# Kernel tuning notes

Measured on AMD Instinct MI355X. Metric: run time of the kernel, lower is better.

The kernel has to match this reference:

```python
import jax, jax.numpy as jnp
import numpy as np
from jax import lax

B, CIN, D = 1, 32, 80      # batch, input channels (diffusion volumes), cube side
CE, CH, COUT = 64, 256, 6  # encoding feats, hidden feats, output feats (DTI components)
N = 200000                 # number of masked voxels
K = 3                      # FOVin


def _conv3d(x, w, b):
    # x: [B,C,D,H,W], w: [O,I,3,3,3], zero padding 1 (matches Conv3d(k=3, pad=1))
    y = lax.conv_general_dilated(x, w, window_strides=(1, 1, 1),
                                 padding=[(K // 2, K // 2)] * 3,
                                 dimension_numbers=('NCDHW', 'OIDHW', 'NCDHW'))
    return y + b[None, :, None, None, None]


def _conv1x1(x, w, b):
    # pointwise Conv1d: x [B,C,N], w [O,C], b [O]
    return jnp.einsum('oc,bcn->bon', w, x) + b[None, :, None]


def setup_inputs() -> dict:
    key = jax.random.key(0)
    ks = jax.random.split(key, 16)
    s3 = 1.0 / np.sqrt(CIN * K ** 3)
    return {
        'img_block': jax.random.normal(ks[0], (B, CIN, D, D, D), jnp.float32),
        'coords0': jax.random.randint(ks[1], (1, N), 0, D, jnp.int32),
        'coords1': jax.random.randint(ks[2], (1, N), 0, D, jnp.int32),
        'coords2': jax.random.randint(ks[3], (1, N), 0, D, jnp.int32),
        # encoder Conv3d weights (kaiming-ish scale)
        'w_enc1': jax.random.normal(ks[4], (CE, CIN, K, K, K), jnp.float32) * s3,
        'b_enc1': jax.random.normal(ks[5], (CE,), jnp.float32) * 0.01,
        'w_enc2': jax.random.normal(ks[6], (CE, CE, K, K, K), jnp.float32) * (1.0 / np.sqrt(CE * K ** 3)),
        'b_enc2': jax.random.normal(ks[7], (CE,), jnp.float32) * 0.01,
        # process stack 1x1 Conv1d weights
        'w_p1': jax.random.normal(ks[8], (CH, CE), jnp.float32) * (1.0 / np.sqrt(CE)),
        'b_p1': jax.random.normal(ks[9], (CH,), jnp.float32) * 0.01,
        'w_p2': jax.random.normal(ks[10], (CH, CH), jnp.float32) * (1.0 / np.sqrt(CH)),
        'b_p2': jax.random.normal(ks[11], (CH,), jnp.float32) * 0.01,
        'w_p3': jax.random.normal(ks[12], (64, CH), jnp.float32) * (1.0 / np.sqrt(CH)),
        'b_p3': jax.random.normal(ks[13], (64,), jnp.float32) * 0.01,
        'w_p4': jax.random.normal(ks[14], (COUT, 64), jnp.float32) * (1.0 / np.sqrt(64)),
        'b_p4': jax.random.normal(ks[15], (COUT,), jnp.float32) * 0.01,
    }


def reference(img_block, coords0, coords1, coords2,
              w_enc1, b_enc1, w_enc2, b_enc2,
              w_p1, b_p1, w_p2, b_p2, w_p3, b_p3, w_p4, b_p4):
    relu = jax.nn.relu
    # net_extrafea: two Conv3d(k=3,pad=1)+ReLU
    f = relu(_conv3d(img_block, w_enc1, b_enc1))
    f = relu(_conv3d(f, w_enc2, b_enc2))          # [B, CE, D, D, D]
    # gather masked voxels -> [B, CE, N]
    g = f[:, :, coords0[0], coords1[0], coords2[0]]
    # net_process (Dropout = identity in eval mode):
    h = relu(_conv1x1(g, w_p1, b_p1))             # [B, CH, N]
    h = relu(_conv1x1(h, w_p2, b_p2))             # [B, CH, N]
    # outermost_linear head: Conv1d(CH->64) then Conv1d(64->COUT), no nonlinearity
    h = _conv1x1(h, w_p3, b_p3)                   # [B, 64, N]
    out = _conv1x1(h, w_p4, b_p4)                 # [B, COUT, N]
    return out
```

## Files before the change

### kernel.cpp

```cpp
#include <hip/hip_runtime.h>
#include <hip/hip_bf16.h>

#define DD 80
#define CIN 32
#define PLANE (DD*DD)
#define VOX (DD*DD*DD)
#define NPTS 200000

typedef __attribute__((ext_vector_type(8))) short bf16x8;
typedef __attribute__((ext_vector_type(4))) float floatx4;
typedef __attribute__((ext_vector_type(4))) short s4v;

static __device__ __forceinline__ short f2bf(float v) {
    __hip_bfloat16 b = __float2bfloat16(v);
    return *(short*)&b;
}

static __device__ __forceinline__ void async_copy16(void* lds, const void* g) {
    __builtin_amdgcn_global_load_lds(
        (const __attribute__((address_space(1))) unsigned int*)g,
        (__attribute__((address_space(3))) unsigned int*)lds, 16, 0, 0);
}

__global__ void convert_weights(const float* __restrict__ w2,
                                const float* __restrict__ w_p1,
                                const float* __restrict__ w_p2,
                                const float* __restrict__ w_p3,
                                const float* __restrict__ w_e1,
                                short* __restrict__ wpb, short* __restrict__ w1f,
                                short* __restrict__ w2f, short* __restrict__ w3f,
                                short* __restrict__ wc1) {
    int i = blockIdx.x * 256 + threadIdx.x;
    if (i < 110592) {
        int off = i >> 12, r = i & 4095;
        int nt = r >> 10, r2 = r & 1023;
        int ks = r2 >> 9, r3 = r2 & 511;
        int lane = r3 >> 3, e = r3 & 7;
        int oc = nt * 16 + (lane & 15);
        int ic = ks * 32 + (lane >> 4) * 8 + e;
        wpb[i] = f2bf(w2[oc * 1728 + ic * 27 + off]);
    } else if (i < 110592 + 16384) {
        int j = i - 110592;
        int frag = j >> 9, r3 = j & 511;
        int lane = r3 >> 3, e = r3 & 7;
        int ks = frag & 1, nt = (frag >> 1) & 3, w = frag >> 3;
        int n = w * 64 + nt * 16 + (lane & 15);
        int k = ks * 32 + (lane >> 4) * 8 + e;
        w1f[j] = f2bf(w_p1[n * 64 + k]);
    } else if (i < 110592 + 16384 + 65536) {
        int j = i - 110592 - 16384;
        int frag = j >> 9, r3 = j & 511;
        int lane = r3 >> 3, e = r3 & 7;
        int ks = frag & 7, nt = (frag >> 3) & 3, w = frag >> 5;
        int n = w * 64 + nt * 16 + (lane & 15);
        int k = ks * 32 + (lane >> 4) * 8 + e;
        w2f[j] = f2bf(w_p2[n * 256 + k]);
    } else if (i < 110592 + 16384 + 65536 + 16384) {
        int j = i - 110592 - 16384 - 65536;
        int frag = j >> 9, r3 = j & 511;
        int lane = r3 >> 3, e = r3 & 7;
        int ks = frag & 7, w = frag >> 3;
        int n = w * 16 + (lane & 15);
        int k = ks * 32 + (lane >> 4) * 8 + e;
        w3f[j] = f2bf(w_p3[n * 256 + k]);
    } else if (i < 110592 + 16384 + 65536 + 16384 + 55296) {
        int j = i - (110592 + 16384 + 65536 + 16384);
        int off = j / 2048, r = j - off * 2048;
        int oc = r >> 5, ic = r & 31;
        wc1[j] = f2bf(w_e1[(oc * 32 + ic) * 27 + off]);
    }
}

__global__ __launch_bounds__(256) void transpose_img(
    const float* __restrict__ img, short* __restrict__ img_t)
{
    int v = blockIdx.x * 256 + threadIdx.x;
    if (v >= VOX) return;
    short row[32];
    #pragma unroll
    for (int ic = 0; ic < 32; ic++)
        row[ic] = f2bf(img[(size_t)ic * VOX + v]);
    int4* dst = (int4*)(img_t + (size_t)v * 32);
    #pragma unroll
    for (int c = 0; c < 4; c++) dst[c] = ((int4*)row)[c];
}

__global__ __launch_bounds__(256) void conv1_mfma(
    const short* __restrict__ img_t, const short* __restrict__ wc1,
    const float* __restrict__ b1, const short* __restrict__ zeros,
    short* __restrict__ f1)
{
    __shared__ short Alds[3072 * 16 / 2];

    const int bh = blockIdx.x;
    const int d = bh / DD, h = bh - d * DD;
    const int tid = threadIdx.x;
    const int w = tid >> 6, lane = tid & 63;
    const int q = lane >> 4, lc = lane & 15;

    for (int i = 0; i < 12; i++) {
        int s = (w * 12 + i) * 64 + lane;
        int row = s >> 2, c = s & 3;
        int cs = c ^ ((row >> 1) & 3);
        int rr = row / 82, v = row - rr * 82;
        int dz = rr / 3, dyy = rr - dz * 3;
        int zz = d + dz - 1, yy = h + dyy - 1, ww = v - 1;
        const short* src = zeros;
        if (row < 738 && (unsigned)zz < DD && (unsigned)yy < DD && (unsigned)ww < DD)
            src = img_t + ((size_t)(zz * PLANE + yy * DD + ww)) * 32 + cs * 8;
        async_copy16(&Alds[(w * 12 + i) * 512], src);
    }
    __syncthreads();

    floatx4 acc[5];
    #pragma unroll
    for (int mt = 0; mt < 5; mt++) acc[mt] = (floatx4){0.f, 0.f, 0.f, 0.f};

    for (int dz = 0; dz < 3; dz++) {
        for (int dy = 0; dy < 3; dy++) {
            const int rr = dz * 3 + dy;
            #pragma unroll
            for (int dx = 0; dx < 3; dx++) {
                const int off = rr * 3 + dx;
                bf16x8 bfr = *(const bf16x8*)(wc1 + ((off * 64 + w * 16 + lc) << 5) + q * 8);
                #pragma unroll
                for (int mt = 0; mt < 5; mt++) {
                    const int vv = rr * 82 + mt * 16 + lc + dx;
                    bf16x8 afr = *(const bf16x8*)(
                        &Alds[vv * 32 + ((q ^ ((vv >> 1) & 3)) << 3)]);
                    acc[mt] = __builtin_amdgcn_mfma_f32_16x16x32_bf16(afr, bfr, acc[mt], 0, 0, 0);
                }
            }
        }
    }

    const int oc = w * 16 + lc;
    const float bias = b1[oc];
    const size_t vbase = (size_t)(d * DD + h) * DD;
    #pragma unroll
    for (int mt = 0; mt < 5; mt++) {
        #pragma unroll
        for (int r = 0; r < 4; r++) {
            const int m = mt * 16 + q * 4 + r;
            float v = acc[mt][r] + bias;
            f1[(vbase + m) * 64 + oc] = f2bf(v > 0.f ? v : 0.f);
        }
    }
}

#define NSB 32

__global__ __launch_bounds__(512) void hist_cells(
    const int* __restrict__ c0, const int* __restrict__ c1, const int* __restrict__ c2,
    int* __restrict__ partial)
{
    __shared__ int h[1000];
    const int tid = threadIdx.x;
    for (int c = tid; c < 1000; c += 512) h[c] = 0;
    __syncthreads();
    for (int p = blockIdx.x * 512 + tid; p < NPTS; p += NSB * 512) {
        int cell = (c0[p] >> 3) * 100 + (c1[p] >> 3) * 10 + (c2[p] >> 3);
        atomicAdd(&h[cell], 1);
    }
    __syncthreads();
    for (int c = tid; c < 1000; c += 512) partial[c * NSB + blockIdx.x] = h[c];
}

__global__ __launch_bounds__(1024) void scan_cells(
    const int* __restrict__ partial, int* __restrict__ blockbase,
    int* __restrict__ cs, int* __restrict__ ce)
{
    __shared__ int a[1024], b[1024];
    const int t = threadIdx.x;
    int sum = 0;
    if (t < 1000) {
        const int base = t * NSB;
        int run = 0;
        #pragma unroll 8
        for (int bb = 0; bb < NSB; bb++) {
            blockbase[base + bb] = run;
            run += partial[base + bb];
        }
        sum = run;
    }
    a[t] = sum;
    __syncthreads();
    int* src = a; int* dst = b;
    for (int d = 1; d < 1024; d <<= 1) {
        int v = src[t];
        if (t >= d) v += src[t - d];
        dst[t] = v;
        __syncthreads();
        int* tmp = src; src = dst; dst = tmp;
    }
    if (t < 1000) { cs[t] = src[t] - sum; ce[t] = src[t]; }
}

__global__ __launch_bounds__(512) void scatter_points(
    const int* __restrict__ c0, const int* __restrict__ c1, const int* __restrict__ c2,
    const int* __restrict__ cs, const int* __restrict__ blockbase,
    int* __restrict__ perm, int* __restrict__ pcoord)
{
    __shared__ int cur[1000];
    const int tid = threadIdx.x;
    for (int c = tid; c < 1000; c += 512) cur[c] = 0;
    __syncthreads();
    for (int p = blockIdx.x * 512 + tid; p < NPTS; p += NSB * 512) {
        int z = c0[p], y = c1[p], x = c2[p];
        int cell = (z >> 3) * 100 + (y >> 3) * 10 + (x >> 3);
        int r = atomicAdd(&cur[cell], 1);
        int pos = cs[cell] + blockbase[cell * NSB + blockIdx.x] + r;
        perm[pos] = p;
        pcoord[pos] = z | (y << 8) | (x << 16);
    }
}

__global__ __launch_bounds__(512) void conv2_halo(
    const short* __restrict__ f1s, const short* __restrict__ wfb,
    const float* __restrict__ b2,
    const int* __restrict__ cs, const int* __restrict__ ce,
    const int* __restrict__ perm, const int* __restrict__ pcoord,
    const short* __restrict__ zeros,
    __hip_bfloat16* __restrict__ g)
{
    __shared__ short Alds[1000 * 64];

    int bid = blockIdx.x;
    { const int xcd = bid & 7, i = bid >> 3; bid = xcd * 125 + i; }
    const int cell = bid;
    const int cz = cell / 100, cyx = cell - cz * 100;
    const int cy = cyx / 10, cx = cyx - cy * 10;

    const int tid = threadIdx.x;
    const int w = tid >> 6, lane = tid & 63;
    const int q = lane >> 4, lc = lane & 15;

    const int pstart = cs[cell], pend = ce[cell];

    const int pr = lane >> 3, pcs = lane & 7, ccs = pcs ^ pr;
    const int gz0 = cz * 8 - 1, gy0 = cy * 8 - 1, gx0 = cx * 8 - 1;
    for (int j = w; j < 125; j += 8) {
        int r = j * 8 + pr;
        int hz = r / 100; int rem = r - hz * 100;
        int hy = rem / 10; int hx = rem - hy * 10;
        int gz = gz0 + hz, gy = gy0 + hy, gx = gx0 + hx;
        const short* src = zeros + ccs * 8;
        if ((unsigned)gz < DD && (unsigned)gy < DD && (unsigned)gx < DD)
            src = f1s + (size_t)(gz * PLANE + gy * DD + gx) * 64 + ccs * 8;
        async_copy16(&Alds[j * 512], src);
    }
    asm volatile("s_waitcnt vmcnt(0)" ::: "memory");
    __syncthreads();

    float bias[4];
    #pragma unroll
    for (int nt = 0; nt < 4; nt++) bias[nt] = b2[nt * 16 + lc];

    for (int pb2 = pstart; pb2 < pend; pb2 += 256) {
        int hbase[2];
        #pragma unroll
        for (int mt = 0; mt < 2; mt++) {
            int p = pb2 + w * 32 + mt * 16 + lc;
            if (p >= pend) p = pend - 1;
            int pk = pcoord[p];
            int z = pk & 0xff, y = (pk >> 8) & 0xff, x = (pk >> 16) & 0xff;
            hbase[mt] = (z - gz0) * 100 + (y - gy0) * 10 + (x - gx0);
        }

        floatx4 acc[2][4];
        #pragma unroll
        for (int mt = 0; mt < 2; mt++)
            #pragma unroll
            for (int nt = 0; nt < 4; nt++)
                acc[mt][nt] = (floatx4){0.f, 0.f, 0.f, 0.f};

        #pragma unroll 3
        for (int off = 0; off < 27; ++off) {
            const int dz = off / 9, rem = off - dz * 9;
            const int dy = rem / 3, dx = rem - dy * 3;
            const int dh = (dz - 1) * 100 + (dy - 1) * 10 + (dx - 1);

            bf16x8 bfr[4][2];
            #pragma unroll
            for (int nt = 0; nt < 4; nt++)
                #pragma unroll
                for (int ks = 0; ks < 2; ks++)
                    bfr[nt][ks] = *(const bf16x8*)(
                        wfb + off * 4096 + nt * 1024 + ks * 512 + lane * 8);

            bf16x8 afr[2][2];
            #pragma unroll
            for (int mt = 0; mt < 2; mt++) {
                const int hrow = hbase[mt] + dh;
                const int sw = hrow & 7;
                #pragma unroll
                for (int ks = 0; ks < 2; ks++)
                    afr[mt][ks] = *(const bf16x8*)(
                        &Alds[hrow * 64 + (((ks * 4 + q) ^ sw) << 3)]);
            }

            #pragma unroll
            for (int ks = 0; ks < 2; ks++)
                #pragma unroll
                for (int mt = 0; mt < 2; mt++)
                    #pragma unroll
                    for (int nt = 0; nt < 4; nt++)
                        acc[mt][nt] = __builtin_amdgcn_mfma_f32_16x16x32_bf16(
                            afr[mt][ks], bfr[nt][ks], acc[mt][nt], 0, 0, 0);
        }

        #pragma unroll
        for (int mt = 0; mt < 2; mt++) {
            const int pt = pb2 + w * 32 + mt * 16 + q * 4;
            #pragma unroll
            for (int r = 0; r < 4; r++) {
                if (pt + r < pend) {
                    const int orig = perm[pt + r];
                    #pragma unroll
                    for (int nt = 0; nt < 4; nt++) {
                        const int oc = nt * 16 + lc;
                        float v = acc[mt][nt][r] + bias[nt];
                        g[(size_t)orig * 64 + oc] = __float2bfloat16(v > 0.f ? v : 0.f);
                    }
                }
            }
        }
    }
}

__global__ __launch_bounds__(256) void mlp_mfma(
    const __hip_bfloat16* __restrict__ g,
    const short* __restrict__ w1f, const float* __restrict__ bp1,
    const short* __restrict__ w2f, const float* __restrict__ bp2,
    const short* __restrict__ w3f, const float* __restrict__ bp3,
    const float* __restrict__ wp4, const float* __restrict__ bp4,
    float* __restrict__ out)
{
    __shared__ short Xls[64 * 64];
    __shared__ short Hb[2][64 * 256];
    float* h3f = (float*)Hb[0];

    const int tid = threadIdx.x;
    const int pb = blockIdx.x * 64;
    const int w = tid >> 6, lane = tid & 63;
    const int q = lane >> 4, lc = lane & 15;

    const short* gs = (const short*)g;
    #pragma unroll
    for (int it = 0; it < 2; it++) {
        int idx = it * 256 + tid;
        int r = idx >> 3, c = idx & 7;
        int4 v = *(const int4*)(gs + (size_t)(pb + r) * 64 + c * 8);
        *(int4*)(&Xls[r * 64 + (c ^ (r & 7)) * 8]) = v;
    }
    __syncthreads();

    {
        floatx4 acc[4][4];
        #pragma unroll
        for (int mt = 0; mt < 4; mt++)
            #pragma unroll
            for (int nt = 0; nt < 4; nt++)
                acc[mt][nt] = (floatx4){0.f, 0.f, 0.f, 0.f};

        #pragma unroll
        for (int ks = 0; ks < 2; ks++) {
            bf16x8 wf[4];
            #pragma unroll
            for (int nt = 0; nt < 4; nt++)
                wf[nt] = *(const bf16x8*)(w1f + (((w * 4 + nt) * 2 + ks) << 9) + lane * 8);
            const int c = ks * 4 + q;
            #pragma unroll
            for (int mt = 0; mt < 4; mt++) {
                const int m = mt * 16 + lc;
                bf16x8 hf = *(const bf16x8*)(&Xls[m * 64 + ((c ^ (m & 7)) << 3)]);
                #pragma unroll
                for (int nt = 0; nt < 4; nt++)
                    acc[mt][nt] = __builtin_amdgcn_mfma_f32_16x16x32_bf16(wf[nt], hf, acc[mt][nt], 0, 0, 0);
            }
        }
        #pragma unroll
        for (int nt = 0; nt < 4; nt++) {
            const floatx4 bs = *(const floatx4*)(bp1 + w * 64 + nt * 16 + q * 4);
            const int chunk = w * 8 + nt * 2 + (q >> 1);
            #pragma unroll
            for (int mt = 0; mt < 4; mt++) {
                const int m = mt * 16 + lc;
                s4v hv;
                #pragma unroll
                for (int r = 0; r < 4; r++) {
                    float v = acc[mt][nt][r] + bs[r];
                    hv[r] = f2bf(v > 0.f ? v : 0.f);
                }
                *(s4v*)(&Hb[0][m * 256 + ((chunk ^ (m & 7)) << 3) + ((q & 1) << 2)]) = hv;
            }
        }
    }
    __syncthreads();

    {
        floatx4 acc[4][4];
        #pragma unroll
        for (int mt = 0; mt < 4; mt++)
            #pragma unroll
            for (int nt = 0; nt < 4; nt++)
                acc[mt][nt] = (floatx4){0.f, 0.f, 0.f, 0.f};

        #pragma unroll
        for (int ks = 0; ks < 8; ks++) {
            bf16x8 wf[4];
            #pragma unroll
            for (int nt = 0; nt < 4; nt++)
                wf[nt] = *(const bf16x8*)(w2f + (((w * 4 + nt) * 8 + ks) << 9) + lane * 8);
            const int c = ks * 4 + q;
            #pragma unroll
            for (int mt = 0; mt < 4; mt++) {
                const int m = mt * 16 + lc;
                bf16x8 hf = *(const bf16x8*)(&Hb[0][m * 256 + ((c ^ (m & 7)) << 3)]);
                #pragma unroll
                for (int nt = 0; nt < 4; nt++)
                    acc[mt][nt] = __builtin_amdgcn_mfma_f32_16x16x32_bf16(wf[nt], hf, acc[mt][nt], 0, 0, 0);
            }
        }
        #pragma unroll
        for (int nt = 0; nt < 4; nt++) {
            const floatx4 bs = *(const floatx4*)(bp2 + w * 64 + nt * 16 + q * 4);
            const int chunk = w * 8 + nt * 2 + (q >> 1);
            #pragma unroll
            for (int mt = 0; mt < 4; mt++) {
                const int m = mt * 16 + lc;
                s4v hv;
                #pragma unroll
                for (int r = 0; r < 4; r++) {
                    float v = acc[mt][nt][r] + bs[r];
                    hv[r] = f2bf(v > 0.f ? v : 0.f);
                }
                *(s4v*)(&Hb[1][m * 256 + ((chunk ^ (m & 7)) << 3) + ((q & 1) << 2)]) = hv;
            }
        }
    }
    __syncthreads();

    {
        floatx4 acc3[4];
        #pragma unroll
        for (int mt = 0; mt < 4; mt++) acc3[mt] = (floatx4){0.f, 0.f, 0.f, 0.f};

        #pragma unroll
        for (int ks = 0; ks < 8; ks++) {
            bf16x8 wf = *(const bf16x8*)(w3f + (((w * 8 + ks)) << 9) + lane * 8);
            const int c = ks * 4 + q;
            #pragma unroll
            for (int mt = 0; mt < 4; mt++) {
                const int m = mt * 16 + lc;
                bf16x8 hf = *(const bf16x8*)(&Hb[1][m * 256 + ((c ^ (m & 7)) << 3)]);
                acc3[mt] = __builtin_amdgcn_mfma_f32_16x16x32_bf16(wf, hf, acc3[mt], 0, 0, 0);
            }
        }
        const floatx4 bs = *(const floatx4*)(bp3 + w * 16 + q * 4);
        __syncthreads();
        #pragma unroll
        for (int mt = 0; mt < 4; mt++) {
            const int m = mt * 16 + lc;
            floatx4 hv;
            #pragma unroll
            for (int r = 0; r < 4; r++) hv[r] = acc3[mt][r] + bs[r];
            *(floatx4*)(&h3f[m * 68 + w * 16 + q * 4]) = hv;
        }
    }
    __syncthreads();

    for (int e = tid; e < 384; e += 256) {
        int c = e >> 6, p = e & 63;
        float a = bp4[c];
        const float* wr = wp4 + c * 64;
        const float* xr = h3f + p * 68;
        #pragma unroll 8
        for (int k = 0; k < 64; k++) a += wr[k] * xr[k];
        out[(size_t)c * NPTS + pb + p] = a;
    }
}

extern "C" void kernel_launch(void* const* d_in, const int* in_sizes, int n_in,
                              void* d_out, int out_size, void* d_ws, size_t ws_size,
                              hipStream_t stream) {
    const float* img = (const float*)d_in[0];
    const int* c0 = (const int*)d_in[1];
    const int* c1 = (const int*)d_in[2];
    const int* c2 = (const int*)d_in[3];
    const float* w_enc1 = (const float*)d_in[4];
    const float* b_enc1 = (const float*)d_in[5];
    const float* w_enc2 = (const float*)d_in[6];
    const float* b_enc2 = (const float*)d_in[7];
    const float* w_p1 = (const float*)d_in[8];
    const float* b_p1 = (const float*)d_in[9];
    const float* w_p2 = (const float*)d_in[10];
    const float* b_p2 = (const float*)d_in[11];
    const float* w_p3 = (const float*)d_in[12];
    const float* b_p3 = (const float*)d_in[13];
    const float* w_p4 = (const float*)d_in[14];
    const float* b_p4 = (const float*)d_in[15];
    float* out = (float*)d_out;

    short* f1b = (short*)d_ws;
    short* wpb = f1b + (size_t)VOX * 64;
    short* w1b = wpb + 110592;
    short* w2b = w1b + 16384;
    short* w3b = w2b + 65536;
    short* gb  = w3b + 16384;
    short* img_t = gb + (size_t)NPTS * 64;
    short* wc1 = img_t + (size_t)VOX * 32;
    short* zeros = wc1 + 55296;

    int* perm      = (int*)img_t;
    int* pcoord    = perm + NPTS;
    int* partial   = pcoord + NPTS;
    int* blockbase = partial + NSB * 1000;
    int* cstart    = blockbase + NSB * 1000;
    int* cend      = cstart + 1000;

    hipMemsetAsync(zeros, 0, 128, stream);
    convert_weights<<<(264192 + 255) / 256, 256, 0, stream>>>(
        w_enc2, w_p1, w_p2, w_p3, w_enc1, wpb, w1b, w2b, w3b, wc1);
    transpose_img<<<(VOX + 255) / 256, 256, 0, stream>>>(img, img_t);
    conv1_mfma<<<DD * DD, 256, 0, stream>>>(img_t, wc1, b_enc1, zeros, f1b);

    hist_cells<<<NSB, 512, 0, stream>>>(c0, c1, c2, partial);
    scan_cells<<<1, 1024, 0, stream>>>(partial, blockbase, cstart, cend);
    scatter_points<<<NSB, 512, 0, stream>>>(c0, c1, c2, cstart, blockbase, perm, pcoord);

    conv2_halo<<<1000, 512, 0, stream>>>(
        f1b, wpb, b_enc2, cstart, cend, perm, pcoord, zeros, (__hip_bfloat16*)gb);
    mlp_mfma<<<NPTS / 64, 256, 0, stream>>>(
        (const __hip_bfloat16*)gb, w1b, b_p1, w2b, b_p2, w3b, b_p3, w_p4, b_p4, out);
}
```

Before: 377.6 us.

## Fuse conv2 halo kernel with MLP stack, reusing shared memory per cell

Merges the sparse conv2 kernel and the pointwise MLP into one per-cell kernel. The conv2 outputs stay in LDS as MLP inputs and final results are scattered to the original point indices through perm, so the bf16 intermediate g never goes to global memory and one launch is removed. Because LDS is shared between the halo tile and the MLP buffers, the halo is reloaded for every 256-point chunk. Per-cell work becomes serialized with many barriers, and cells with many points pay for repeated halo loads. The MFMA operand order in conv2 is swapped to fit the new output layout.

Result: slower. 409.7 us (+8.5%).

```diff
diff --git a/kernel.cpp b/kernel.cpp
--- a/kernel.cpp
+++ b/kernel.cpp
@@ -215,15 +215,24 @@
     }
 }
 
-__global__ __launch_bounds__(512) void conv2_halo(
+__global__ __launch_bounds__(512) void conv2_mlp_fused(
     const short* __restrict__ f1s, const short* __restrict__ wfb,
     const float* __restrict__ b2,
     const int* __restrict__ cs, const int* __restrict__ ce,
     const int* __restrict__ perm, const int* __restrict__ pcoord,
     const short* __restrict__ zeros,
-    __hip_bfloat16* __restrict__ g)
+    const short* __restrict__ w1f, const float* __restrict__ bp1,
+    const short* __restrict__ w2f, const float* __restrict__ bp2,
+    const short* __restrict__ w3f, const float* __restrict__ bp3,
+    const float* __restrict__ wp4, const float* __restrict__ bp4,
+    float* __restrict__ out)
 {
-    __shared__ short Alds[1000 * 64];
+    __shared__ short U[64000];
+    short* Alds = U;
+    short* Xg = U;
+    short* H1 = U + 16384;
+    short* H2 = U + 32768;
+    float* h3f = (float*)H1;
 
     int bid = blockIdx.x;
     { const int xcd = bid & 7, i = bid >> 3; bid = xcd * 125 + i; }
@@ -236,27 +245,23 @@
     const int q = lane >> 4, lc = lane & 15;
 
     const int pstart = cs[cell], pend = ce[cell];
-
     const int pr = lane >> 3, pcs = lane & 7, ccs = pcs ^ pr;
     const int gz0 = cz * 8 - 1, gy0 = cy * 8 - 1, gx0 = cx * 8 - 1;
-    for (int j = w; j < 125; j += 8) {
-        int r = j * 8 + pr;
-        int hz = r / 100; int rem = r - hz * 100;
-        int hy = rem / 10; int hx = rem - hy * 10;
-        int gz = gz0 + hz, gy = gy0 + hy, gx = gx0 + hx;
-        const short* src = zeros + ccs * 8;
-        if ((unsigned)gz < DD && (unsigned)gy < DD && (unsigned)gx < DD)
-            src = f1s + (size_t)(gz * PLANE + gy * DD + gx) * 64 + ccs * 8;
-        async_copy16(&Alds[j * 512], src);
-    }
-    asm volatile("s_waitcnt vmcnt(0)" ::: "memory");
-    __syncthreads();
-
-    float bias[4];
-    #pragma unroll
-    for (int nt = 0; nt < 4; nt++) bias[nt] = b2[nt * 16 + lc];
 
     for (int pb2 = pstart; pb2 < pend; pb2 += 256) {
+        for (int j = w; j < 125; j += 8) {
+            int r = j * 8 + pr;
+            int hz = r / 100; int rem = r - hz * 100;
+            int hy = rem / 10; int hx = rem - hy * 10;
+            int gz = gz0 + hz, gy = gy0 + hy, gx = gx0 + hx;
+            const short* src = zeros + ccs * 8;
+            if ((unsigned)gz < DD && (unsigned)gy < DD && (unsigned)gx < DD)
+                src = f1s + (size_t)(gz * PLANE + gy * DD + gx) * 64 + ccs * 8;
+            async_copy16(&Alds[j * 512], src);
+        }
+        asm volatile("s_waitcnt vmcnt(0)" ::: "memory");
+        __syncthreads();
+
         int hbase[2];
         #pragma unroll
         for (int mt = 0; mt < 2; mt++) {
@@ -274,210 +279,206 @@
             for (int nt = 0; nt < 4; nt++)
                 acc[mt][nt] = (floatx4){0.f, 0.f, 0.f, 0.f};
 
-        #pragma unroll 3
-        for (int off = 0; off < 27; ++off) {
-            const int dz = off / 9, rem = off - dz * 9;
-            const int dy = rem / 3, dx = rem - dy * 3;
-            const int dh = (dz - 1) * 100 + (dy - 1) * 10 + (dx - 1);
-
-            bf16x8 bfr[4][2];
+        if (pb2 + w * 32 < pend) {
+            for (int dz = 0; dz < 3; dz++) {
+                for (int dy = 0; dy < 3; dy++) {
+                    const int rowoff = (dz - 1) * 100 + (dy - 1) * 10;
+                    const int offbase = (dz * 3 + dy) * 3;
+                    #pragma unroll
+                    for (int dx = 0; dx < 3; dx++) {
+                        const int off = offbase + dx;
+                        const int dh = rowoff + dx - 1;
+
+                        bf16x8 bfr[4][2];
+                        #pragma unroll
+                        for (int nt = 0; nt < 4; nt++)
+                            #pragma unroll
+                            for (int ks = 0; ks < 2; ks++)
+                                bfr[nt][ks] = *(const bf16x8*)(
+                                    wfb + off * 4096 + nt * 1024 + ks * 512 + lane * 8);
+
+                        bf16x8 afr[2][2];
+                        #pragma unroll
+                        for (int mt = 0; mt < 2; mt++) {
+                            const int hrow = hbase[mt] + dh;
+                            const int sw = hrow & 7;
+                            #pragma unroll
+                            for (int ks = 0; ks < 2; ks++)
+                                afr[mt][ks] = *(const bf16x8*)(
+                                    &Alds[hrow * 64 + (((ks * 4 + q) ^ sw) << 3)]);
+                        }
+
+                        #pragma unroll
+                        for (int ks = 0; ks < 2; ks++)
+                            #pragma unroll
+                            for (int mt = 0; mt < 2; mt++)
+                                #pragma unroll
+                                for (int nt = 0; nt < 4; nt++)
+                                    acc[mt][nt] = __builtin_amdgcn_mfma_f32_16x16x32_bf16(
+                                        bfr[nt][ks], afr[mt][ks], acc[mt][nt], 0, 0, 0);
+                    }
+                }
+            }
+        }
+        __syncthreads();
+
+        {
+            short* Xw = Xg + (w >> 1) * 4096;
             #pragma unroll
-            for (int nt = 0; nt < 4; nt++)
-                #pragma unroll
-                for (int ks = 0; ks < 2; ks++)
-                    bfr[nt][ks] = *(const bf16x8*)(
-                        wfb + off * 4096 + nt * 1024 + ks * 512 + lane * 8);
-
-            bf16x8 afr[2][2];
-            #pragma unroll
-            for (int mt = 0; mt < 2; mt++) {
-                const int hrow = hbase[mt] + dh;
-                const int sw = hrow & 7;
-                #pragma unroll
-                for (int ks = 0; ks < 2; ks++)
-                    afr[mt][ks] = *(const bf16x8*)(
-                        &Alds[hrow * 64 + (((ks * 4 + q) ^ sw) << 3)]);
-            }
-
-            #pragma unroll
-            for (int ks = 0; ks < 2; ks++)
-                #pragma unroll
-                for (int mt = 0; mt < 2; mt++)
-                    #pragma unroll
-                    for (int nt = 0; nt < 4; nt++)
-                        acc[mt][nt] = __builtin_amdgcn_mfma_f32_16x16x32_bf16(
-                            afr[mt][ks], bfr[nt][ks], acc[mt][nt], 0, 0, 0);
-        }
-
-        #pragma unroll
-        for (int mt = 0; mt < 2; mt++) {
-            const int pt = pb2 + w * 32 + mt * 16 + q * 4;
-            #pragma unroll
-            for (int r = 0; r < 4; r++) {
-                if (pt + r < pend) {
-                    const int orig = perm[pt + r];
-                    #pragma unroll
-                    for (int nt = 0; nt < 4; nt++) {
-                        const int oc = nt * 16 + lc;
-                        float v = acc[mt][nt][r] + bias[nt];
-                        g[(size_t)orig * 64 + oc] = __float2bfloat16(v > 0.f ? v : 0.f);
-                    }
-                }
-            }
-        }
-    }
-}
-
-__global__ __launch_bounds__(256) void mlp_mfma(
-    const __hip_bfloat16* __restrict__ g,
-    const short* __restrict__ w1f, const float* __restrict__ bp1,
-    const short* __restrict__ w2f, const float* __restrict__ bp2,
-    const short* __restrict__ w3f, const float* __restrict__ bp3,
-    const float* __restrict__ wp4, const float* __restrict__ bp4,
-    float* __restrict__ out)
-{
-    __shared__ short Xls[64 * 64];
-    __shared__ short Hb[2][64 * 256];
-    float* h3f = (float*)Hb[0];
-
-    const int tid = threadIdx.x;
-    const int pb = blockIdx.x * 64;
-    const int w = tid >> 6, lane = tid & 63;
-    const int q = lane >> 4, lc = lane & 15;
-
-    const short* gs = (const short*)g;
-    #pragma unroll
-    for (int it = 0; it < 2; it++) {
-        int idx = it * 256 + tid;
-        int r = idx >> 3, c = idx & 7;
-        int4 v = *(const int4*)(gs + (size_t)(pb + r) * 64 + c * 8);
-        *(int4*)(&Xls[r * 64 + (c ^ (r & 7)) * 8]) = v;
-    }
-    __syncthreads();
-
-    {
-        floatx4 acc[4][4];
-        #pragma unroll
-        for (int mt = 0; mt < 4; mt++)
-            #pragma unroll
-            for (int nt = 0; nt < 4; nt++)
-                acc[mt][nt] = (floatx4){0.f, 0.f, 0.f, 0.f};
-
-        #pragma unroll
-        for (int ks = 0; ks < 2; ks++) {
-            bf16x8 wf[4];
-            #pragma unroll
-            for (int nt = 0; nt < 4; nt++)
-                wf[nt] = *(const bf16x8*)(w1f + (((w * 4 + nt) * 2 + ks) << 9) + lane * 8);
-            const int c = ks * 4 + q;
-            #pragma unroll
-            for (int mt = 0; mt < 4; mt++) {
-                const int m = mt * 16 + lc;
-                bf16x8 hf = *(const bf16x8*)(&Xls[m * 64 + ((c ^ (m & 7)) << 3)]);
-                #pragma unroll
-                for (int nt = 0; nt < 4; nt++)
-                    acc[mt][nt] = __builtin_amdgcn_mfma_f32_16x16x32_bf16(wf[nt], hf, acc[mt][nt], 0, 0, 0);
-            }
-        }
-        #pragma unroll
-        for (int nt = 0; nt < 4; nt++) {
-            const floatx4 bs = *(const floatx4*)(bp1 + w * 64 + nt * 16 + q * 4);
-            const int chunk = w * 8 + nt * 2 + (q >> 1);
-            #pragma unroll
-            for (int mt = 0; mt < 4; mt++) {
-                const int m = mt * 16 + lc;
-                s4v hv;
-                #pragma unroll
-                for (int r = 0; r < 4; r++) {
-                    float v = acc[mt][nt][r] + bs[r];
-                    hv[r] = f2bf(v > 0.f ? v : 0.f);
-                }
-                *(s4v*)(&Hb[0][m * 256 + ((chunk ^ (m & 7)) << 3) + ((q & 1) << 2)]) = hv;
-            }
-        }
-    }
-    __syncthreads();
-
-    {
-        floatx4 acc[4][4];
-        #pragma unroll
-        for (int mt = 0; mt < 4; mt++)
-            #pragma unroll
-            for (int nt = 0; nt < 4; nt++)
-                acc[mt][nt] = (floatx4){0.f, 0.f, 0.f, 0.f};
-
-        #pragma unroll
-        for (int ks = 0; ks < 8; ks++) {
-            bf16x8 wf[4];
-            #pragma unroll
-            for (int nt = 0; nt < 4; nt++)
-                wf[nt] = *(const bf16x8*)(w2f + (((w * 4 + nt) * 8 + ks) << 9) + lane * 8);
-            const int c = ks * 4 + q;
-            #pragma unroll
-            for (int mt = 0; mt < 4; mt++) {
-                const int m = mt * 16 + lc;
-                bf16x8 hf = *(const bf16x8*)(&Hb[0][m * 256 + ((c ^ (m & 7)) << 3)]);
-                #pragma unroll
-                for (int nt = 0; nt < 4; nt++)
-                    acc[mt][nt] = __builtin_amdgcn_mfma_f32_16x16x32_bf16(wf[nt], hf, acc[mt][nt], 0, 0, 0);
-            }
-        }
-        #pragma unroll
-        for (int nt = 0; nt < 4; nt++) {
-            const floatx4 bs = *(const floatx4*)(bp2 + w * 64 + nt * 16 + q * 4);
-            const int chunk = w * 8 + nt * 2 + (q >> 1);
-            #pragma unroll
-            for (int mt = 0; mt < 4; mt++) {
-                const int m = mt * 16 + lc;
-                s4v hv;
-                #pragma unroll
-                for (int r = 0; r < 4; r++) {
-                    float v = acc[mt][nt][r] + bs[r];
-                    hv[r] = f2bf(v > 0.f ? v : 0.f);
-                }
-                *(s4v*)(&Hb[1][m * 256 + ((chunk ^ (m & 7)) << 3) + ((q & 1) << 2)]) = hv;
-            }
-        }
-    }
-    __syncthreads();
-
-    {
-        floatx4 acc3[4];
-        #pragma unroll
-        for (int mt = 0; mt < 4; mt++) acc3[mt] = (floatx4){0.f, 0.f, 0.f, 0.f};
-
-        #pragma unroll
-        for (int ks = 0; ks < 8; ks++) {
-            bf16x8 wf = *(const bf16x8*)(w3f + (((w * 8 + ks)) << 9) + lane * 8);
-            const int c = ks * 4 + q;
-            #pragma unroll
-            for (int mt = 0; mt < 4; mt++) {
-                const int m = mt * 16 + lc;
-                bf16x8 hf = *(const bf16x8*)(&Hb[1][m * 256 + ((c ^ (m & 7)) << 3)]);
-                acc3[mt] = __builtin_amdgcn_mfma_f32_16x16x32_bf16(wf, hf, acc3[mt], 0, 0, 0);
-            }
-        }
-        const floatx4 bs = *(const floatx4*)(bp3 + w * 16 + q * 4);
+            for (int nt = 0; nt < 4; nt++) {
+                const floatx4 bs = *(const floatx4*)(b2 + nt * 16 + q * 4);
+                const int chunk = nt * 2 + (q >> 1);
+                #pragma unroll
+                for (int mt = 0; mt < 2; mt++) {
+                    const int m = (w & 1) * 32 + mt * 16 + lc;
+                    s4v hv;
+                    #pragma unroll
+                    for (int r = 0; r < 4; r++) {
+                        float v = acc[mt][nt][r] + bs[r];
+                        hv[r] = f2bf(v > 0.f ? v : 0.f);
+                    }
+                    *(s4v*)(&Xw[m * 64 + ((chunk ^ (m & 7)) << 3) + ((q & 1) << 2)]) = hv;
+                }
+            }
+        }
         __syncthreads();
-        #pragma unroll
-        for (int mt = 0; mt < 4; mt++) {
-            const int m = mt * 16 + lc;
-            floatx4 hv;
-            #pragma unroll
-            for (int r = 0; r < 4; r++) hv[r] = acc3[mt][r] + bs[r];
-            *(floatx4*)(&h3f[m * 68 + w * 16 + q * 4]) = hv;
-        }
-    }
-    __syncthreads();
-
-    for (int e = tid; e < 384; e += 256) {
-        int c = e >> 6, p = e & 63;
-        float a = bp4[c];
-        const float* wr = wp4 + c * 64;
-        const float* xr = h3f + p * 68;
-        #pragma unroll 8
-        for (int k = 0; k < 64; k++) a += wr[k] * xr[k];
-        out[(size_t)c * NPTS + pb + p] = a;
+
+        for (int grp = 0; grp < 4; grp++) {
+            if (pb2 + grp * 64 >= pend) break;
+            const short* Xls = Xg + grp * 4096;
+
+            {
+                floatx4 a1[4][2];
+                #pragma unroll
+                for (int mt = 0; mt < 4; mt++)
+                    #pragma unroll
+                    for (int j = 0; j < 2; j++)
+                        a1[mt][j] = (floatx4){0.f, 0.f, 0.f, 0.f};
+
+                #pragma unroll
+                for (int ks = 0; ks < 2; ks++) {
+                    bf16x8 wf[2];
+                    #pragma unroll
+                    for (int j = 0; j < 2; j++)
+                        wf[j] = *(const bf16x8*)(w1f + (((2 * w + j) * 2 + ks) << 9) + lane * 8);
+                    const int c = ks * 4 + q;
+                    #pragma unroll
+                    for (int mt = 0; mt < 4; mt++) {
+                        const int m = mt * 16 + lc;
+                        bf16x8 hf = *(const bf16x8*)(&Xls[m * 64 + ((c ^ (m & 7)) << 3)]);
+                        #pragma unroll
+                        for (int j = 0; j < 2; j++)
+                            a1[mt][j] = __builtin_amdgcn_mfma_f32_16x16x32_bf16(wf[j], hf, a1[mt][j], 0, 0, 0);
+                    }
+                }
+                #pragma unroll
+                for (int j = 0; j < 2; j++) {
+                    const int nidx = 2 * w + j;
+                    const floatx4 bs = *(const floatx4*)(bp1 + nidx * 16 + q * 4);
+                    const int chunk = nidx * 2 + (q >> 1);
+                    #pragma unroll
+                    for (int mt = 0; mt < 4; mt++) {
+                        const int m = mt * 16 + lc;
+                        s4v hv;
+                        #pragma unroll
+                        for (int r = 0; r < 4; r++) {
+                            float v = a1[mt][j][r] + bs[r];
+                            hv[r] = f2bf(v > 0.f ? v : 0.f);
+                        }
+                        *(s4v*)(&H1[m * 256 + ((chunk ^ (m & 7)) << 3) + ((q & 1) << 2)]) = hv;
+                    }
+                }
+            }
+            __syncthreads();
+
+            {
+                floatx4 a2[4][2];
+                #pragma unroll
+                for (int mt = 0; mt < 4; mt++)
+                    #pragma unroll
+                    for (int j = 0; j < 2; j++)
+                        a2[mt][j] = (floatx4){0.f, 0.f, 0.f, 0.f};
+
+                #pragma unroll
+                for (int ks = 0; ks < 8; ks++) {
+                    bf16x8 wf[2];
+                    #pragma unroll
+                    for (int j = 0; j < 2; j++)
+                        wf[j] = *(const bf16x8*)(w2f + (((2 * w + j) * 8 + ks) << 9) + lane * 8);
+                    const int c = ks * 4 + q;
+                    #pragma unroll
+                    for (int mt = 0; mt < 4; mt++) {
+                        const int m = mt * 16 + lc;
+                        bf16x8 hf = *(const bf16x8*)(&H1[m * 256 + ((c ^ (m & 7)) << 3)]);
+                        #pragma unroll
+                        for (int j = 0; j < 2; j++)
+                            a2[mt][j] = __builtin_amdgcn_mfma_f32_16x16x32_bf16(wf[j], hf, a2[mt][j], 0, 0, 0);
+                    }
+                }
+                __syncthreads();
+                #pragma unroll
+                for (int j = 0; j < 2; j++) {
+                    const int nidx = 2 * w + j;
+                    const floatx4 bs = *(const floatx4*)(bp2 + nidx * 16 + q * 4);
+                    const int chunk = nidx * 2 + (q >> 1);
+                    #pragma unroll
+                    for (int mt = 0; mt < 4; mt++) {
+                        const int m = mt * 16 + lc;
+                        s4v hv;
+                        #pragma unroll
+                        for (int r = 0; r < 4; r++) {
+                            float v = a2[mt][j][r] + bs[r];
+                            hv[r] = f2bf(v > 0.f ? v : 0.f);
+                        }
+                        *(s4v*)(&H2[m * 256 + ((chunk ^ (m & 7)) << 3) + ((q & 1) << 2)]) = hv;
+                    }
+                }
+            }
+            __syncthreads();
+
+            {
+                floatx4 a3[4];
+                #pragma unroll
+                for (int mt = 0; mt < 4; mt++) a3[mt] = (floatx4){0.f, 0.f, 0.f, 0.f};
+                if (w < 4) {
+                    #pragma unroll
+                    for (int ks = 0; ks < 8; ks++) {
+                        bf16x8 wf = *(const bf16x8*)(w3f + ((w * 8 + ks) << 9) + lane * 8);
+                        const int c = ks * 4 + q;
+                        #pragma unroll
+                        for (int mt = 0; mt < 4; mt++) {
+                            const int m = mt * 16 + lc;
+                            bf16x8 hf = *(const bf16x8*)(&H2[m * 256 + ((c ^ (m & 7)) << 3)]);
+                            a3[mt] = __builtin_amdgcn_mfma_f32_16x16x32_bf16(wf, hf, a3[mt], 0, 0, 0);
+                        }
+                    }
+                    const floatx4 bs = *(const floatx4*)(bp3 + w * 16 + q * 4);
+                    #pragma unroll
+                    for (int mt = 0; mt < 4; mt++) {
+                        const int m = mt * 16 + lc;
+                        floatx4 hv;
+                        #pragma unroll
+                        for (int r = 0; r < 4; r++) hv[r] = a3[mt][r] + bs[r];
+                        *(floatx4*)(&h3f[m * 68 + w * 16 + q * 4]) = hv;
+                    }
+                }
+            }
+            __syncthreads();
+
+            for (int e = tid; e < 384; e += 512) {
+                int c = e >> 6, p = e & 63;
+                int gp = pb2 + grp * 64 + p;
+                if (gp < pend) {
+                    float a = bp4[c];
+                    const float* wr = wp4 + c * 64;
+                    const float* xr = h3f + p * 68;
+                    #pragma unroll 8
+                    for (int k = 0; k < 64; k++) a += wr[k] * xr[k];
+                    out[(size_t)c * NPTS + perm[gp]] = a;
+                }
+            }
+            __syncthreads();
+        }
     }
 }
 
@@ -529,8 +530,7 @@
     scan_cells<<<1, 1024, 0, stream>>>(partial, blockbase, cstart, cend);
     scatter_points<<<NSB, 512, 0, stream>>>(c0, c1, c2, cstart, blockbase, perm, pcoord);
 
-    conv2_halo<<<1000, 512, 0, stream>>>(
-        f1b, wpb, b_enc2, cstart, cend, perm, pcoord, zeros, (__hip_bfloat16*)gb);
-    mlp_mfma<<<NPTS / 64, 256, 0, stream>>>(
-        (const __hip_bfloat16*)gb, w1b, b_p1, w2b, b_p2, w3b, b_p3, w_p4, b_p4, out);
-}
+    conv2_mlp_fused<<<1000, 512, 0, stream>>>(
+        f1b, wpb, b_enc2, cstart, cend, perm, pcoord, zeros,
+        w1b, b_p1, w2b, b_p2, w3b, b_p3, w_p4, b_p4, out);
+}
```
